# Kernel optimization log

Hardware: AMD Instinct MI355X
Metric: run time of the kernel (lower is better)

The kernel has to match this reference:

```python
import jax, jax.numpy as jnp
import numpy as np

HIDDEN = 512
EPS = 1e-5


def conv2d(x, w, pad):
    # x: (N, Cin, H, W), w: (Cout, Cin, kh, kw)
    return jax.lax.conv_general_dilated(
        x, w, window_strides=(1, 1), padding=[(pad, pad), (pad, pad)],
        dimension_numbers=("NCHW", "OIHW", "NCHW"))


def setup_inputs() -> dict:
    key = jax.random.key(0)
    ks = jax.random.split(key, 8)
    B, Cin, H, W = 256, 2304, 7, 7
    fan = lambda w: w.shape[1] * w.shape[2] * w.shape[3]
    def wconv(k, shape):
        w = jax.random.normal(k, shape, dtype=jnp.float32)
        return w * (1.0 / np.sqrt(shape[1] * shape[2] * shape[3]))
    return {
        "status": jax.random.normal(ks[0], (B, 2), dtype=jnp.float32),
        "rois": jax.random.uniform(ks[1], (B, 2), dtype=jnp.float32),
        "bbox_featx": jax.random.normal(ks[2], (B, Cin, 1, H, W), dtype=jnp.float32),
        "w_reduce": wconv(ks[3], (HIDDEN, Cin, 3, 3)),
        "w_q": wconv(ks[4], (HIDDEN, 2, 3, 3)),
        "w_k": wconv(ks[5], (HIDDEN, HIDDEN, 3, 3)),
        "w_v": wconv(ks[6], (HIDDEN, HIDDEN, 3, 3)),
        "w_out": wconv(ks[7], (HIDDEN, HIDDEN, 3, 3)),
        "gamma": jnp.ones((HIDDEN,), dtype=jnp.float32),
        "beta": jnp.zeros((HIDDEN,), dtype=jnp.float32),
    }


def reference(status, rois, bbox_featx, w_reduce, w_q, w_k, w_v, w_out, gamma, beta):
    x = bbox_featx[:, :, 0]                      # (B, Cin, H, W)
    x = conv2d(x, w_reduce, 1)                   # (B, C, H, W)
    B, C, H, W = x.shape
    st = jnp.concatenate([status[:, :1], rois[:, 1:]], axis=1)  # (B, 2)
    st = jnp.broadcast_to(st[:, :, None, None], (B, st.shape[1], H, W))
    q = conv2d(st, w_q, 1)                       # (B, C, H, W)
    k = conv2d(x, w_k, 1)                        # (B, C, H, W)
    v = conv2d(x, w_v, 1)                        # (B, C, H, W)
    # batch-wise attention: att[b, j, h, w] = sum_c q[b,c,h,w] * k[j,c,h,w]
    att = jnp.einsum("bchw,jchw->bjhw", q, k) / jnp.sqrt(jnp.float32(C))
    att = jax.nn.softmax(att, axis=1)            # softmax over key index j
    virt = jnp.einsum("bjhw,jchw->bchw", att, v) # weighted V sum
    # GroupNorm(1 group): normalize over (C, H, W) per sample
    mu = jnp.mean(virt, axis=(1, 2, 3), keepdims=True)
    var = jnp.var(virt, axis=(1, 2, 3), keepdims=True)
    virt = (virt - mu) / jnp.sqrt(var + EPS)
    virt = virt * gamma[None, :, None, None] + beta[None, :, None, None]
    virt = jax.nn.relu(virt)
    virt = conv2d(virt, w_out, 1)
    # dropout is identity in eval mode
    out = x + virt
    return out[:, :, None]                       # (B, C, 1, H, W)
```

## Files before the change

### kernel.cpp

```cpp
#include <hip/hip_runtime.h>
#include <stdint.h>

#define AS1 __attribute__((address_space(1)))
#define AS3 __attribute__((address_space(3)))

typedef __bf16 bf16x8 __attribute__((ext_vector_type(8)));
typedef float  f32x4  __attribute__((ext_vector_type(4)));

__device__ __forceinline__ void gl_lds16(const void* g, void* l) {
    __builtin_amdgcn_global_load_lds((AS1 void*)g, (AS3 void*)l, 16, 0, 0);
}

__device__ __forceinline__ ushort f2bf(float f) {
    unsigned x = __float_as_uint(f);
    return (ushort)((x + 0x7fffu + ((x >> 16) & 1u)) >> 16);
}

template <int AMODE, int EPI>
__global__ __launch_bounds__(256, 4) void gemm_bt(
    const ushort* __restrict__ A, const ushort* __restrict__ BT,
    float* __restrict__ OF, ushort* __restrict__ OU0, ushort* __restrict__ OU1,
    int M, int N, int K, int Cin, int Ksegs, int splitZ) {
    __shared__ ushort As[128 * 64];
    __shared__ ushort Bs[128 * 64];

    const int t = threadIdx.x;
    const int lane = t & 63;
    const int wave = t >> 6;
    const int wm = wave & 1, wn = wave >> 1;
    const int blockN = blockIdx.x * 128;
    const int blockM = blockIdx.y * 128;
    const int z = blockIdx.z;

    const char* Ab = (const char*)A;
    const char* Bb = (const char*)BT;
    if (AMODE == 0) {
        Ab += (size_t)z * (size_t)M * (size_t)K * 2;
        Bb += (size_t)z * (size_t)N * (size_t)K * 2;
    }

    const int rS = t >> 2;
    const int seg = (t & 3) * 16;

    unsigned abase0, abase1;
    if (AMODE == 1) {
        int m0 = blockM + rS, m1 = m0 + 64;
        int b0 = m0 / 49, p0 = m0 % 49;
        int b1 = m1 / 49, p1 = m1 % 49;
        abase0 = (unsigned)(((b0 * 9 + p0 / 7) * 9 + p0 % 7) * Cin);
        abase1 = (unsigned)(((b1 * 9 + p1 / 7) * 9 + p1 % 7) * Cin);
    } else {
        abase0 = (unsigned)((blockM + rS) * K);
        abase1 = abase0 + (unsigned)(64 * K);
    }
    const unsigned bbase0 = (unsigned)((blockN + rS) * K);
    const unsigned bbase1 = bbase0 + (unsigned)(64 * K);

    f32x4 zero = {0.f, 0.f, 0.f, 0.f};
    f32x4 acc[4][4];
    for (int i = 0; i < 4; i++)
        for (int j = 0; j < 4; j++) acc[i][j] = zero;

    const unsigned chunk = (AMODE == 1) ? (unsigned)(Cin / splitZ) : (unsigned)K;
    const unsigned ciBase = (AMODE == 1) ? (unsigned)z * chunk : 0u;
    const int citers2 = (int)(chunk / 64);
    const int nseg = (AMODE == 1) ? Ksegs : 1;

    for (int s = 0; s < nseg; ++s) {
        const char *aseg0, *aseg1, *bseg0, *bseg1;
        if (AMODE == 1) {
            unsigned shift = (unsigned)(((s / 3) * 9 + (s % 3)) * Cin) + ciBase;
            aseg0 = Ab + (size_t)(abase0 + shift) * 2 + seg;
            aseg1 = Ab + (size_t)(abase1 + shift) * 2 + seg;
            unsigned bshift = (unsigned)(s * Cin) + ciBase;
            bseg0 = Bb + (size_t)(bbase0 + bshift) * 2 + seg;
            bseg1 = Bb + (size_t)(bbase1 + bshift) * 2 + seg;
        } else {
            aseg0 = Ab + (size_t)abase0 * 2 + seg;
            aseg1 = Ab + (size_t)abase1 * 2 + seg;
            bseg0 = Bb + (size_t)bbase0 * 2 + seg;
            bseg1 = Bb + (size_t)bbase1 * 2 + seg;
        }

        for (int ct = 0; ct < citers2; ++ct) {
            const int o0 = ct * 128;
            const int o1 = ct * 128 + 64;
            __syncthreads();
            gl_lds16(aseg0 + o0, (char*)As + t * 16);
            gl_lds16(aseg1 + o0, (char*)As + 4096 + t * 16);
            gl_lds16(bseg0 + o0, (char*)Bs + t * 16);
            gl_lds16(bseg1 + o0, (char*)Bs + 4096 + t * 16);
            gl_lds16(aseg0 + o1, (char*)As + 8192 + t * 16);
            gl_lds16(aseg1 + o1, (char*)As + 12288 + t * 16);
            gl_lds16(bseg0 + o1, (char*)Bs + 8192 + t * 16);
            gl_lds16(bseg1 + o1, (char*)Bs + 12288 + t * 16);
            __syncthreads();

#pragma unroll
            for (int h = 0; h < 2; ++h) {
                const ushort* Ap = As + h * 4096 + (wm * 64 + (lane & 15)) * 32 + (lane >> 4) * 8;
                const ushort* Bp = Bs + h * 4096 + (wn * 64 + (lane & 15)) * 32 + (lane >> 4) * 8;
                bf16x8 af[4], bfr[4];
#pragma unroll
                for (int i = 0; i < 4; i++) {
                    af[i] = *(const bf16x8*)(Ap + i * 16 * 32);
                    bfr[i] = *(const bf16x8*)(Bp + i * 16 * 32);
                }
#pragma unroll
                for (int i = 0; i < 4; i++)
#pragma unroll
                    for (int j = 0; j < 4; j++)
                        acc[i][j] = __builtin_amdgcn_mfma_f32_16x16x32_bf16(af[i], bfr[j], acc[i][j], 0, 0, 0);
            }
        }
    }

    const int mrow = (lane >> 4) * 4;
    const int ncol = lane & 15;
#pragma unroll
    for (int i = 0; i < 4; i++) {
#pragma unroll
        for (int j = 0; j < 4; j++) {
            f32x4 v = acc[i][j];
#pragma unroll
            for (int r = 0; r < 4; r++) {
                int m = blockM + wm * 64 + i * 16 + mrow + r;
                int n = blockN + wn * 64 + j * 16 + ncol;
                float val = v[r];
                if (EPI == 0) {
                    OF[((size_t)z * M + m) * N + n] = val;
                } else if (EPI == 1) {
                    int j2 = m / 49, p = m % 49;
                    if (n < 512)
                        OU0[(size_t)(p * 256 + j2) * 512 + n] = f2bf(val);
                    else
                        OU1[(size_t)(p * 256 + j2) * 512 + (n - 512)] = f2bf(val);
                } else if (EPI == 2) {
                    OF[((size_t)z * 256 + m) * 256 + n] = val;
                } else {
                    OF[((size_t)z * 256 + m) * 512 + n] = val;
                }
            }
        }
    }
}

__global__ void border_k(ushort* __restrict__ base, int C, int nvec) {
    int id = blockIdx.x * 256 + threadIdx.x;
    if (id >= nvec) return;
    int cpc = C >> 2;
    int c4 = (id % cpc) * 4;
    int r = id / cpc;
    int cell = r & 31, b = r >> 5;
    int hp, wp;
    if (cell < 9) { hp = 0; wp = cell; }
    else if (cell < 18) { hp = 8; wp = cell - 9; }
    else { int e2 = cell - 18; hp = 1 + (e2 >> 1); wp = (e2 & 1) ? 8 : 0; }
    ushort4 zz = {0, 0, 0, 0};
    *(ushort4*)(base + ((size_t)(b * 9 + hp) * 9 + wp) * C + c4) = zz;
}

__global__ __launch_bounds__(256) void reduce1_k(const float* __restrict__ P,
                                                 float* __restrict__ XF, ushort* __restrict__ xp) {
    __shared__ float lf[256 * 49];
    int h = blockIdx.x, b = blockIdx.y, t = threadIdx.x;
    const float* p0 = P + ((size_t)b * 49) * 512 + h * 256;
    const float* p1 = p0 + (size_t)12544 * 512;
    for (int e = t; e < 49 * 64; e += 256) {
        int p = e >> 6, c4 = (e & 63) << 2;
        float4 a = *(const float4*)(p0 + (size_t)p * 512 + c4);
        float4 c = *(const float4*)(p1 + (size_t)p * 512 + c4);
        a.x += c.x; a.y += c.y; a.z += c.z; a.w += c.w;
        ushort4 u;
        u.x = f2bf(a.x); u.y = f2bf(a.y); u.z = f2bf(a.z); u.w = f2bf(a.w);
        *(ushort4*)(xp + (size_t)((b * 9 + p / 7 + 1) * 9 + p % 7 + 1) * 512 + h * 256 + c4) = u;
        lf[(c4 + 0) * 49 + p] = a.x;
        lf[(c4 + 1) * 49 + p] = a.y;
        lf[(c4 + 2) * 49 + p] = a.z;
        lf[(c4 + 3) * 49 + p] = a.w;
    }
    __syncthreads();
    float* xfb = XF + (size_t)b * 25088 + h * 12544;
    for (int e = t; e < 256 * 49; e += 256) xfb[e] = lf[e];
}

__global__ __launch_bounds__(256) void reduce2_k(const float* __restrict__ P,
                                                 const float* __restrict__ XF, float* __restrict__ out) {
    __shared__ float lf[256 * 49];
    int h = blockIdx.x, b = blockIdx.y, t = threadIdx.x;
    const float* p0 = P + ((size_t)b * 49) * 512 + h * 256;
    const float* p1 = p0 + (size_t)12544 * 512;
    for (int e = t; e < 49 * 64; e += 256) {
        int p = e >> 6, c4 = (e & 63) << 2;
        float4 a = *(const float4*)(p0 + (size_t)p * 512 + c4);
        float4 c = *(const float4*)(p1 + (size_t)p * 512 + c4);
        lf[(c4 + 0) * 49 + p] = a.x + c.x;
        lf[(c4 + 1) * 49 + p] = a.y + c.y;
        lf[(c4 + 2) * 49 + p] = a.z + c.z;
        lf[(c4 + 3) * 49 + p] = a.w + c.w;
    }
    __syncthreads();
    const float* xfb = XF + (size_t)b * 25088 + h * 12544;
    float* ob = out + (size_t)b * 25088 + h * 12544;
    for (int e = t; e < 256 * 49; e += 256) ob[e] = xfb[e] + lf[e];
}

__global__ __launch_bounds__(256) void cast_x0_k(const float* __restrict__ in, ushort* __restrict__ out) {
    __shared__ ushort tl[576 * 49];
    int cit = blockIdx.x, b = blockIdx.y, t = threadIdx.x;
    const float* src = in + ((size_t)b * 2304 + cit * 576) * 49;
    for (int e4 = t; e4 < 7056; e4 += 256) {
        float4 v = *(const float4*)(src + e4 * 4);
        ushort4 u;
        u.x = f2bf(v.x); u.y = f2bf(v.y); u.z = f2bf(v.z); u.w = f2bf(v.w);
        *(ushort4*)(tl + e4 * 4) = u;
    }
    __syncthreads();
    for (int e4 = t; e4 < 7056; e4 += 256) {
        int p = e4 / 144, c4 = (e4 % 144) * 4;
        ushort4 u;
        u.x = tl[c4 * 49 + p]; u.y = tl[(c4 + 1) * 49 + p];
        u.z = tl[(c4 + 2) * 49 + p]; u.w = tl[(c4 + 3) * 49 + p];
        *(ushort4*)(out + (size_t)((b * 9 + p / 7 + 1) * 9 + p % 7 + 1) * 2304 + cit * 576 + c4) = u;
    }
}

__global__ void cast_w_k(const float* __restrict__ in, ushort* __restrict__ out, int Cin) {
    __shared__ float lds[256 * 9];
    int co = blockIdx.x, t = threadIdx.x;
    for (int ci0 = 0; ci0 < Cin; ci0 += 256) {
        const float* src = in + ((size_t)co * Cin + ci0 + t) * 9;
#pragma unroll
        for (int j = 0; j < 9; j++) lds[t * 9 + j] = src[j];
        __syncthreads();
#pragma unroll
        for (int s = 0; s < 9; s++) out[((size_t)co * 9 + s) * Cin + ci0 + t] = f2bf(lds[t * 9 + s]);
        __syncthreads();
    }
}

__global__ void wsq_k(const float* __restrict__ wq, float* __restrict__ WSQ) {
    int p = blockIdx.x, co = threadIdx.x;
    int h = p / 7, w = p % 7;
#pragma unroll
    for (int ci = 0; ci < 2; ci++) {
        float a = 0.f;
        for (int kh = 0; kh < 3; kh++) {
            int hi = h + kh - 1;
            if (hi < 0 || hi > 6) continue;
            for (int kw = 0; kw < 3; kw++) {
                int wi = w + kw - 1;
                if (wi < 0 || wi > 6) continue;
                a += wq[(((size_t)co * 2 + ci) * 3 + kh) * 3 + kw];
            }
        }
        WSQ[((size_t)p * 2 + ci) * 512 + co] = a;
    }
}

__global__ void qgen_k(const float* __restrict__ status, const float* __restrict__ rois,
                       const float* __restrict__ WSQ, ushort* __restrict__ qb) {
    int b = blockIdx.x, p = blockIdx.y, t = threadIdx.x;
    float st0 = status[b * 2], st1 = rois[b * 2 + 1];
    int c = t * 2;
    const float* w0 = WSQ + (size_t)p * 2 * 512;
    const float sc = 0.04419417382415922f;
    float q0 = (st0 * w0[c] + st1 * w0[512 + c]) * sc;
    float q1 = (st0 * w0[c + 1] + st1 * w0[512 + c + 1]) * sc;
    unsigned u = (unsigned)f2bf(q0) | ((unsigned)f2bf(q1) << 16);
    *(unsigned*)(qb + ((size_t)p * 256 + b) * 512 + c) = u;
}

__global__ void softmax_k(const float* __restrict__ S, ushort* __restrict__ att) {
    int row = blockIdx.x * 4 + (threadIdx.x >> 6);
    int lane = threadIdx.x & 63;
    const float4 sv = *(const float4*)(S + (size_t)row * 256 + lane * 4);
    float m = fmaxf(fmaxf(sv.x, sv.y), fmaxf(sv.z, sv.w));
    for (int o = 32; o > 0; o >>= 1) m = fmaxf(m, __shfl_xor(m, o));
    float e0 = __expf(sv.x - m), e1 = __expf(sv.y - m);
    float e2 = __expf(sv.z - m), e3 = __expf(sv.w - m);
    float s = e0 + e1 + e2 + e3;
    for (int o = 32; o > 0; o >>= 1) s += __shfl_xor(s, o);
    float inv = 1.f / s;
    ushort4 o4;
    o4.x = f2bf(e0 * inv); o4.y = f2bf(e1 * inv);
    o4.z = f2bf(e2 * inv); o4.w = f2bf(e3 * inv);
    *(ushort4*)(att + (size_t)row * 256 + lane * 4) = o4;
}

__global__ void transpose_v_k(const ushort* __restrict__ vb, ushort* __restrict__ vt) {
    __shared__ ushort tl[64][66];
    int p = blockIdx.z, j0 = blockIdx.y * 64, c0 = blockIdx.x * 64;
    int t = threadIdx.x;
#pragma unroll
    for (int i = 0; i < 4; i++) {
        int e = i * 1024 + t * 4;
        int j = e >> 6, c = e & 63;
        ushort4 v = *(const ushort4*)(vb + ((size_t)p * 256 + j0 + j) * 512 + c0 + c);
        tl[j][c] = v.x; tl[j][c + 1] = v.y; tl[j][c + 2] = v.z; tl[j][c + 3] = v.w;
    }
    __syncthreads();
#pragma unroll
    for (int i = 0; i < 4; i++) {
        int e = i * 1024 + t * 4;
        int cc = e >> 6, jj = e & 63;
        ushort4 o;
        o.x = tl[jj][cc]; o.y = tl[jj + 1][cc]; o.z = tl[jj + 2][cc]; o.w = tl[jj + 3][cc];
        *(ushort4*)(vt + ((size_t)p * 512 + c0 + cc) * 256 + j0 + jj) = o;
    }
}

__global__ __launch_bounds__(256) void ln_k(const float* __restrict__ virt, const float* __restrict__ gamma,
                                            const float* __restrict__ beta, ushort* __restrict__ vp) {
    int b = blockIdx.x, t = threadIdx.x;
    float s1 = 0.f, s2 = 0.f;
    for (int p = 0; p < 49; p++) {
        const float* r = virt + ((size_t)p * 256 + b) * 512;
        float a = r[t], c = r[t + 256];
        s1 += a + c;
        s2 += a * a + c * c;
    }
    for (int o = 32; o > 0; o >>= 1) { s1 += __shfl_xor(s1, o); s2 += __shfl_xor(s2, o); }
    __shared__ float red[8];
    int wave = t >> 6, lane = t & 63;
    if (lane == 0) { red[wave] = s1; red[4 + wave] = s2; }
    __syncthreads();
    float S1 = red[0] + red[1] + red[2] + red[3];
    float S2 = red[4] + red[5] + red[6] + red[7];
    float mean = S1 * (1.f / 25088.f);
    float var = S2 * (1.f / 25088.f) - mean * mean;
    float rs = rsqrtf(var + 1e-5f);
    float g0 = gamma[t], b0 = beta[t], g1 = gamma[t + 256], b1 = beta[t + 256];
    for (int p = 0; p < 49; p++) {
        const float* r = virt + ((size_t)p * 256 + b) * 512;
        size_t ob = ((size_t)(b * 9 + p / 7 + 1) * 9 + p % 7 + 1) * 512;
        vp[ob + t] = f2bf(fmaxf((r[t] - mean) * rs * g0 + b0, 0.f));
        vp[ob + t + 256] = f2bf(fmaxf((r[t + 256] - mean) * rs * g1 + b1, 0.f));
    }
#pragma unroll
    for (int e = 0; e < 32; e++) {
        int hp, wp;
        if (e < 9) { hp = 0; wp = e; }
        else if (e < 18) { hp = 8; wp = e - 9; }
        else { int e2 = e - 18; hp = 1 + (e2 >> 1); wp = (e2 & 1) ? 8 : 0; }
        size_t ob = ((size_t)(b * 9 + hp) * 9 + wp) * 512;
        vp[ob + t] = 0;
        vp[ob + t + 256] = 0;
    }
}

extern "C" void kernel_launch(void* const* d_in, const int* in_sizes, int n_in,
                              void* d_out, int out_size, void* d_ws, size_t ws_size,
                              hipStream_t stream) {
    const float* status = (const float*)d_in[0];
    const float* rois = (const float*)d_in[1];
    const float* bfeat = (const float*)d_in[2];
    const float* w_red = (const float*)d_in[3];
    const float* w_q = (const float*)d_in[4];
    const float* w_k = (const float*)d_in[5];
    const float* w_v = (const float*)d_in[6];
    const float* w_o = (const float*)d_in[7];
    const float* gamma = (const float*)d_in[8];
    const float* beta = (const float*)d_in[9];
    float* out = (float*)d_out;
    char* ws = (char*)d_ws;

    const size_t OFF_P = 0;
    const size_t OFF_KB = 0;
    const size_t OFF_VB = 12845056;
    const size_t OFF_VT = 25690112;
    const size_t OFF_QB = 38535168;
    const size_t OFF_B = 51380224;
    const size_t OFF_XF = OFF_B;
    const size_t OFF_XPAD = OFF_B + 25690112;
    const size_t OFF_S = OFF_B + 46923776;
    const size_t OFF_ATT = OFF_B + 59768832;
    const size_t OFF_VIRT = OFF_B + 66191360;
    const size_t OFF_W1T = 146931712;
    const size_t OFF_WKVT = OFF_W1T + 21233664;
    const size_t OFF_WOT = OFF_WKVT + 9437184;
    const size_t OFF_WSQ = OFF_WOT + 4718592;
    const size_t NEED = OFF_WSQ + 200704;
    if (ws_size < NEED) return;

    border_k<<<18432, 256, 0, stream>>>((ushort*)(ws + OFF_B), 2304, 256 * 32 * 576);
    cast_x0_k<<<dim3(4, 256), 256, 0, stream>>>(bfeat, (ushort*)(ws + OFF_B));
    cast_w_k<<<512, 256, 0, stream>>>(w_red, (ushort*)(ws + OFF_W1T), 2304);
    cast_w_k<<<512, 256, 0, stream>>>(w_k, (ushort*)(ws + OFF_WKVT), 512);
    cast_w_k<<<512, 256, 0, stream>>>(w_v, (ushort*)(ws + OFF_WKVT) + (size_t)512 * 9 * 512, 512);
    cast_w_k<<<512, 256, 0, stream>>>(w_o, (ushort*)(ws + OFF_WOT), 512);
    gemm_bt<1, 0><<<dim3(4, 98, 2), 256, 0, stream>>>(
        (ushort*)(ws + OFF_B), (ushort*)(ws + OFF_W1T),
        (float*)(ws + OFF_P), nullptr, nullptr,
        12544, 512, 20736, 2304, 9, 2);
    border_k<<<4096, 256, 0, stream>>>((ushort*)(ws + OFF_XPAD), 512, 256 * 32 * 128);
    reduce1_k<<<dim3(2, 256), 256, 0, stream>>>(
        (const float*)(ws + OFF_P), (float*)(ws + OFF_XF), (ushort*)(ws + OFF_XPAD));
    gemm_bt<1, 1><<<dim3(8, 98, 1), 256, 0, stream>>>(
        (ushort*)(ws + OFF_XPAD), (ushort*)(ws + OFF_WKVT),
        nullptr, (ushort*)(ws + OFF_KB), (ushort*)(ws + OFF_VB),
        12544, 1024, 4608, 512, 9, 1);
    wsq_k<<<49, 512, 0, stream>>>(w_q, (float*)(ws + OFF_WSQ));
    qgen_k<<<dim3(256, 49), 256, 0, stream>>>(status, rois, (float*)(ws + OFF_WSQ), (ushort*)(ws + OFF_QB));
    transpose_v_k<<<dim3(8, 4, 49), 256, 0, stream>>>((ushort*)(ws + OFF_VB), (ushort*)(ws + OFF_VT));
    gemm_bt<0, 2><<<dim3(2, 2, 49), 256, 0, stream>>>(
        (ushort*)(ws + OFF_QB), (ushort*)(ws + OFF_KB),
        (float*)(ws + OFF_S), nullptr, nullptr, 256, 256, 512, 512, 1, 1);
    softmax_k<<<3136, 256, 0, stream>>>((float*)(ws + OFF_S), (ushort*)(ws + OFF_ATT));
    gemm_bt<0, 3><<<dim3(4, 2, 49), 256, 0, stream>>>(
        (ushort*)(ws + OFF_ATT), (ushort*)(ws + OFF_VT),
        (float*)(ws + OFF_VIRT), nullptr, nullptr, 256, 512, 256, 256, 1, 1);
    ln_k<<<256, 256, 0, stream>>>((float*)(ws + OFF_VIRT), gamma, beta, (ushort*)(ws + OFF_XPAD));
    gemm_bt<1, 0><<<dim3(4, 98, 2), 256, 0, stream>>>(
        (ushort*)(ws + OFF_XPAD), (ushort*)(ws + OFF_WOT),
        (float*)(ws + OFF_P), nullptr, nullptr,
        12544, 512, 4608, 512, 9, 2);
    reduce2_k<<<dim3(2, 256), 256, 0, stream>>>(
        (const float*)(ws + OFF_P), (const float*)(ws + OFF_XF), out);
}
```

Baseline: 1.092 ms.

## Raise split-K to four with bf16 partial outputs and split KV conv GEMM

The conv GEMMs now use a larger split-K (four slices for the reduce and out convs, two for the fused K/V conv). Each slice writes bf16 partials instead of fp32, and the partials are summed in reduce kernels, including a new reduce_kv_k that also scatters into the K and V layouts. The attention-times-V output and the GroupNorm input also become bf16. The aim is more parallel work per GEMM and less partial-sum memory traffic. The cost is lower accumulation precision, since partials are rounded to bf16 before summing, and one extra reduction kernel.

```diff
diff --git a/kernel.cpp b/kernel.cpp
--- a/kernel.cpp
+++ b/kernel.cpp
@@ -15,11 +15,14 @@
     unsigned x = __float_as_uint(f);
     return (ushort)((x + 0x7fffu + ((x >> 16) & 1u)) >> 16);
 }
+__device__ __forceinline__ float bf2f(ushort u) {
+    return __uint_as_float((unsigned)u << 16);
+}
 
 template <int AMODE, int EPI>
 __global__ __launch_bounds__(256, 4) void gemm_bt(
     const ushort* __restrict__ A, const ushort* __restrict__ BT,
-    float* __restrict__ OF, ushort* __restrict__ OU0, ushort* __restrict__ OU1,
+    float* __restrict__ OF, ushort* __restrict__ OU0,
     int M, int N, int K, int Cin, int Ksegs, int splitZ) {
     __shared__ ushort As[128 * 64];
     __shared__ ushort Bs[128 * 64];
@@ -128,17 +131,11 @@
                 int n = blockN + wn * 64 + j * 16 + ncol;
                 float val = v[r];
                 if (EPI == 0) {
-                    OF[((size_t)z * M + m) * N + n] = val;
-                } else if (EPI == 1) {
-                    int j2 = m / 49, p = m % 49;
-                    if (n < 512)
-                        OU0[(size_t)(p * 256 + j2) * 512 + n] = f2bf(val);
-                    else
-                        OU1[(size_t)(p * 256 + j2) * 512 + (n - 512)] = f2bf(val);
+                    OU0[((size_t)z * M + m) * N + n] = f2bf(val);
                 } else if (EPI == 2) {
                     OF[((size_t)z * 256 + m) * 256 + n] = val;
                 } else {
-                    OF[((size_t)z * 256 + m) * 512 + n] = val;
+                    OU0[((size_t)z * 256 + m) * 512 + n] = f2bf(val);
                 }
             }
         }
@@ -160,49 +157,76 @@
     *(ushort4*)(base + ((size_t)(b * 9 + hp) * 9 + wp) * C + c4) = zz;
 }
 
-__global__ __launch_bounds__(256) void reduce1_k(const float* __restrict__ P,
+__global__ __launch_bounds__(256) void reduce1_k(const ushort* __restrict__ P,
                                                  float* __restrict__ XF, ushort* __restrict__ xp) {
     __shared__ float lf[256 * 49];
     int h = blockIdx.x, b = blockIdx.y, t = threadIdx.x;
-    const float* p0 = P + ((size_t)b * 49) * 512 + h * 256;
-    const float* p1 = p0 + (size_t)12544 * 512;
+    const size_t zs = (size_t)12544 * 512;
+    const ushort* base = P + ((size_t)b * 49) * 512 + h * 256;
     for (int e = t; e < 49 * 64; e += 256) {
         int p = e >> 6, c4 = (e & 63) << 2;
-        float4 a = *(const float4*)(p0 + (size_t)p * 512 + c4);
-        float4 c = *(const float4*)(p1 + (size_t)p * 512 + c4);
-        a.x += c.x; a.y += c.y; a.z += c.z; a.w += c.w;
-        ushort4 u;
-        u.x = f2bf(a.x); u.y = f2bf(a.y); u.z = f2bf(a.z); u.w = f2bf(a.w);
-        *(ushort4*)(xp + (size_t)((b * 9 + p / 7 + 1) * 9 + p % 7 + 1) * 512 + h * 256 + c4) = u;
-        lf[(c4 + 0) * 49 + p] = a.x;
-        lf[(c4 + 1) * 49 + p] = a.y;
-        lf[(c4 + 2) * 49 + p] = a.z;
-        lf[(c4 + 3) * 49 + p] = a.w;
+        float s0 = 0.f, s1 = 0.f, s2 = 0.f, s3 = 0.f;
+#pragma unroll
+        for (int z = 0; z < 4; z++) {
+            ushort4 u = *(const ushort4*)(base + zs * z + (size_t)p * 512 + c4);
+            s0 += bf2f(u.x); s1 += bf2f(u.y); s2 += bf2f(u.z); s3 += bf2f(u.w);
+        }
+        ushort4 o;
+        o.x = f2bf(s0); o.y = f2bf(s1); o.z = f2bf(s2); o.w = f2bf(s3);
+        *(ushort4*)(xp + (size_t)((b * 9 + p / 7 + 1) * 9 + p % 7 + 1) * 512 + h * 256 + c4) = o;
+        lf[(c4 + 0) * 49 + p] = s0;
+        lf[(c4 + 1) * 49 + p] = s1;
+        lf[(c4 + 2) * 49 + p] = s2;
+        lf[(c4 + 3) * 49 + p] = s3;
     }
     __syncthreads();
     float* xfb = XF + (size_t)b * 25088 + h * 12544;
     for (int e = t; e < 256 * 49; e += 256) xfb[e] = lf[e];
 }
 
-__global__ __launch_bounds__(256) void reduce2_k(const float* __restrict__ P,
+__global__ __launch_bounds__(256) void reduce2_k(const ushort* __restrict__ P,
                                                  const float* __restrict__ XF, float* __restrict__ out) {
     __shared__ float lf[256 * 49];
     int h = blockIdx.x, b = blockIdx.y, t = threadIdx.x;
-    const float* p0 = P + ((size_t)b * 49) * 512 + h * 256;
-    const float* p1 = p0 + (size_t)12544 * 512;
+    const size_t zs = (size_t)12544 * 512;
+    const ushort* base = P + ((size_t)b * 49) * 512 + h * 256;
     for (int e = t; e < 49 * 64; e += 256) {
         int p = e >> 6, c4 = (e & 63) << 2;
-        float4 a = *(const float4*)(p0 + (size_t)p * 512 + c4);
-        float4 c = *(const float4*)(p1 + (size_t)p * 512 + c4);
-        lf[(c4 + 0) * 49 + p] = a.x + c.x;
-        lf[(c4 + 1) * 49 + p] = a.y + c.y;
-        lf[(c4 + 2) * 49 + p] = a.z + c.z;
-        lf[(c4 + 3) * 49 + p] = a.w + c.w;
+        float s0 = 0.f, s1 = 0.f, s2 = 0.f, s3 = 0.f;
+#pragma unroll
+        for (int z = 0; z < 4; z++) {
+            ushort4 u = *(const ushort4*)(base + zs * z + (size_t)p * 512 + c4);
+            s0 += bf2f(u.x); s1 += bf2f(u.y); s2 += bf2f(u.z); s3 += bf2f(u.w);
+        }
+        lf[(c4 + 0) * 49 + p] = s0;
+        lf[(c4 + 1) * 49 + p] = s1;
+        lf[(c4 + 2) * 49 + p] = s2;
+        lf[(c4 + 3) * 49 + p] = s3;
     }
     __syncthreads();
     const float* xfb = XF + (size_t)b * 25088 + h * 12544;
     float* ob = out + (size_t)b * 25088 + h * 12544;
     for (int e = t; e < 256 * 49; e += 256) ob[e] = xfb[e] + lf[e];
+}
+
+__global__ void reduce_kv_k(const ushort* __restrict__ P,
+                            ushort* __restrict__ kb, ushort* __restrict__ vb) {
+    int id = blockIdx.x * 256 + threadIdx.x;
+    int n8 = id & 127, m = id >> 7;
+    int b = m / 49, p = m % 49;
+    const ushort* p0 = P + (size_t)m * 1024 + n8 * 8;
+    const ushort* p1 = p0 + (size_t)12544 * 1024;
+    ushort4 a0 = *(const ushort4*)p0, a1 = *(const ushort4*)(p0 + 4);
+    ushort4 b0 = *(const ushort4*)p1, b1 = *(const ushort4*)(p1 + 4);
+    ushort4 o0, o1;
+    o0.x = f2bf(bf2f(a0.x) + bf2f(b0.x)); o0.y = f2bf(bf2f(a0.y) + bf2f(b0.y));
+    o0.z = f2bf(bf2f(a0.z) + bf2f(b0.z)); o0.w = f2bf(bf2f(a0.w) + bf2f(b0.w));
+    o1.x = f2bf(bf2f(a1.x) + bf2f(b1.x)); o1.y = f2bf(bf2f(a1.y) + bf2f(b1.y));
+    o1.z = f2bf(bf2f(a1.z) + bf2f(b1.z)); o1.w = f2bf(bf2f(a1.w) + bf2f(b1.w));
+    size_t dst = ((size_t)p * 256 + b) * 512;
+    ushort* o = (n8 < 64) ? (kb + dst + n8 * 8) : (vb + dst + (n8 - 64) * 8);
+    *(ushort4*)o = o0;
+    *(ushort4*)(o + 4) = o1;
 }
 
 __global__ __launch_bounds__(256) void cast_x0_k(const float* __restrict__ in, ushort* __restrict__ out) {
@@ -310,13 +334,13 @@
     }
 }
 
-__global__ __launch_bounds__(256) void ln_k(const float* __restrict__ virt, const float* __restrict__ gamma,
+__global__ __launch_bounds__(256) void ln_k(const ushort* __restrict__ virt, const float* __restrict__ gamma,
                                             const float* __restrict__ beta, ushort* __restrict__ vp) {
     int b = blockIdx.x, t = threadIdx.x;
     float s1 = 0.f, s2 = 0.f;
     for (int p = 0; p < 49; p++) {
-        const float* r = virt + ((size_t)p * 256 + b) * 512;
-        float a = r[t], c = r[t + 256];
+        const ushort* r = virt + ((size_t)p * 256 + b) * 512;
+        float a = bf2f(r[t]), c = bf2f(r[t + 256]);
         s1 += a + c;
         s2 += a * a + c * c;
     }
@@ -332,10 +356,10 @@
     float rs = rsqrtf(var + 1e-5f);
     float g0 = gamma[t], b0 = beta[t], g1 = gamma[t + 256], b1 = beta[t + 256];
     for (int p = 0; p < 49; p++) {
-        const float* r = virt + ((size_t)p * 256 + b) * 512;
+        const ushort* r = virt + ((size_t)p * 256 + b) * 512;
         size_t ob = ((size_t)(b * 9 + p / 7 + 1) * 9 + p % 7 + 1) * 512;
-        vp[ob + t] = f2bf(fmaxf((r[t] - mean) * rs * g0 + b0, 0.f));
-        vp[ob + t + 256] = f2bf(fmaxf((r[t + 256] - mean) * rs * g1 + b1, 0.f));
+        vp[ob + t] = f2bf(fmaxf((bf2f(r[t]) - mean) * rs * g0 + b0, 0.f));
+        vp[ob + t + 256] = f2bf(fmaxf((bf2f(r[t + 256]) - mean) * rs * g1 + b1, 0.f));
     }
 #pragma unroll
     for (int e = 0; e < 32; e++) {
@@ -366,16 +390,15 @@
     char* ws = (char*)d_ws;
 
     const size_t OFF_P = 0;
-    const size_t OFF_KB = 0;
-    const size_t OFF_VB = 12845056;
-    const size_t OFF_VT = 25690112;
-    const size_t OFF_QB = 38535168;
+    const size_t OFF_QB = 0;
+    const size_t OFF_S = 12845056;
+    const size_t OFF_ATT = 25690112;
     const size_t OFF_B = 51380224;
     const size_t OFF_XF = OFF_B;
     const size_t OFF_XPAD = OFF_B + 25690112;
-    const size_t OFF_S = OFF_B + 46923776;
-    const size_t OFF_ATT = OFF_B + 59768832;
-    const size_t OFF_VIRT = OFF_B + 66191360;
+    const size_t OFF_KB = OFF_B + 46923776;
+    const size_t OFF_VB = OFF_B + 59768832;
+    const size_t OFF_VT = OFF_B + 72613888;
     const size_t OFF_W1T = 146931712;
     const size_t OFF_WKVT = OFF_W1T + 21233664;
     const size_t OFF_WOT = OFF_WKVT + 9437184;
@@ -389,32 +412,34 @@
     cast_w_k<<<512, 256, 0, stream>>>(w_k, (ushort*)(ws + OFF_WKVT), 512);
     cast_w_k<<<512, 256, 0, stream>>>(w_v, (ushort*)(ws + OFF_WKVT) + (size_t)512 * 9 * 512, 512);
     cast_w_k<<<512, 256, 0, stream>>>(w_o, (ushort*)(ws + OFF_WOT), 512);
-    gemm_bt<1, 0><<<dim3(4, 98, 2), 256, 0, stream>>>(
+    wsq_k<<<49, 512, 0, stream>>>(w_q, (float*)(ws + OFF_WSQ));
+    gemm_bt<1, 0><<<dim3(4, 98, 4), 256, 0, stream>>>(
         (ushort*)(ws + OFF_B), (ushort*)(ws + OFF_W1T),
-        (float*)(ws + OFF_P), nullptr, nullptr,
-        12544, 512, 20736, 2304, 9, 2);
+        nullptr, (ushort*)(ws + OFF_P),
+        12544, 512, 20736, 2304, 9, 4);
     border_k<<<4096, 256, 0, stream>>>((ushort*)(ws + OFF_XPAD), 512, 256 * 32 * 128);
     reduce1_k<<<dim3(2, 256), 256, 0, stream>>>(
-        (const float*)(ws + OFF_P), (float*)(ws + OFF_XF), (ushort*)(ws + OFF_XPAD));
-    gemm_bt<1, 1><<<dim3(8, 98, 1), 256, 0, stream>>>(
+        (const ushort*)(ws + OFF_P), (float*)(ws + OFF_XF), (ushort*)(ws + OFF_XPAD));
+    gemm_bt<1, 0><<<dim3(8, 98, 2), 256, 0, stream>>>(
         (ushort*)(ws + OFF_XPAD), (ushort*)(ws + OFF_WKVT),
-        nullptr, (ushort*)(ws + OFF_KB), (ushort*)(ws + OFF_VB),
-        12544, 1024, 4608, 512, 9, 1);
-    wsq_k<<<49, 512, 0, stream>>>(w_q, (float*)(ws + OFF_WSQ));
+        nullptr, (ushort*)(ws + OFF_P),
+        12544, 1024, 4608, 512, 9, 2);
+    reduce_kv_k<<<6272, 256, 0, stream>>>(
+        (const ushort*)(ws + OFF_P), (ushort*)(ws + OFF_KB), (ushort*)(ws + OFF_VB));
+    transpose_v_k<<<dim3(8, 4, 49), 256, 0, stream>>>((ushort*)(ws + OFF_VB), (ushort*)(ws + OFF_VT));
     qgen_k<<<dim3(256, 49), 256, 0, stream>>>(status, rois, (float*)(ws + OFF_WSQ), (ushort*)(ws + OFF_QB));
-    transpose_v_k<<<dim3(8, 4, 49), 256, 0, stream>>>((ushort*)(ws + OFF_VB), (ushort*)(ws + OFF_VT));
     gemm_bt<0, 2><<<dim3(2, 2, 49), 256, 0, stream>>>(
         (ushort*)(ws + OFF_QB), (ushort*)(ws + OFF_KB),
-        (float*)(ws + OFF_S), nullptr, nullptr, 256, 256, 512, 512, 1, 1);
+        (float*)(ws + OFF_S), nullptr, 256, 256, 512, 512, 1, 1);
     softmax_k<<<3136, 256, 0, stream>>>((float*)(ws + OFF_S), (ushort*)(ws + OFF_ATT));
     gemm_bt<0, 3><<<dim3(4, 2, 49), 256, 0, stream>>>(
         (ushort*)(ws + OFF_ATT), (ushort*)(ws + OFF_VT),
-        (float*)(ws + OFF_VIRT), nullptr, nullptr, 256, 512, 256, 256, 1, 1);
-    ln_k<<<256, 256, 0, stream>>>((float*)(ws + OFF_VIRT), gamma, beta, (ushort*)(ws + OFF_XPAD));
-    gemm_bt<1, 0><<<dim3(4, 98, 2), 256, 0, stream>>>(
+        nullptr, (ushort*)(ws + OFF_VB), 256, 512, 256, 256, 1, 1);
+    ln_k<<<256, 256, 0, stream>>>((const ushort*)(ws + OFF_VB), gamma, beta, (ushort*)(ws + OFF_XPAD));
+    gemm_bt<1, 0><<<dim3(4, 98, 4), 256, 0, stream>>>(
         (ushort*)(ws + OFF_XPAD), (ushort*)(ws + OFF_WOT),
-        (float*)(ws + OFF_P), nullptr, nullptr,
-        12544, 512, 4608, 512, 9, 2);
+        nullptr, (ushort*)(ws + OFF_P),
+        12544, 512, 4608, 512, 9, 4);
     reduce2_k<<<dim3(2, 256), 256, 0, stream>>>(
-        (const float*)(ws + OFF_P), (const float*)(ws + OFF_XF), out);
-}
+        (const ushort*)(ws + OFF_P), (const float*)(ws + OFF_XF), out);
+}
```

After: 995.0 us. 1.1x faster.
